# Performance work log

Hardware: AMD Instinct MI355X
Metric: run time of the kernel (lower is better)

The kernel has to match this reference:

```python
import jax, jax.numpy as jnp
import numpy as np
from jax.scipy.special import logsumexp

FEAT = 256; HEADS = 4; HDIM = FEAT // HEADS; LAYERS = 4
CLS = 3; S = 8; H, W = 400, 800; HC, WC = H // S, W // S
POS_FREQ = 10; VERTEX_THRESH = 0.015; BN_EPS = 1e-5
D_IN = 2 + 4 * POS_FREQ + 1 + CLS * S * S  # 235


def conv1d(x, Wt, b):
    # pointwise Conv1d: x [b,Cin,N] -> [b,Cout,N]
    return jnp.einsum('oi,bin->bon', Wt, x) + b[None, :, None]


def bnorm(x, p):
    # eval-mode BatchNorm1d over channel axis; p = stack([gamma,beta,mean,var]) [4,C]
    g, bt, mu, var = p[0], p[1], p[2], p[3]
    return g[None, :, None] * (x - mu[None, :, None]) * jax.lax.rsqrt(var[None, :, None] + BN_EPS) + bt[None, :, None]


def simple_nms(s, r):
    # max-pool NMS exactly as torch simple_nms (2 suppression rounds)
    def mp(x):
        return jax.lax.reduce_window(x, -jnp.inf, jax.lax.max,
                                     (1, 2 * r + 1, 2 * r + 1), (1, 1, 1), 'SAME')
    zeros = jnp.zeros_like(s)
    max_mask = s == mp(s)
    for _ in range(2):
        supp = mp(max_mask.astype(s.dtype)) > 0
        ss = jnp.where(supp, zeros, s)
        new_max = ss == mp(ss)
        max_mask = max_mask | (new_max & (~supp))
    return jnp.where(max_mask, s, zeros)


def pos_embed(nv):
    freqs = 2.0 ** jnp.linspace(0.0, POS_FREQ - 1.0, POS_FREQ)
    ang = nv[..., None, :] * freqs[None, None, :, None]          # [b,k,Pf,2]
    sc = jnp.concatenate([jnp.sin(ang), jnp.cos(ang)], -1)       # [b,k,Pf,4]
    return jnp.concatenate([nv, sc.reshape(nv.shape[0], nv.shape[1], -1)], -1)


def log_optimal_transport(scores, alpha, iters):
    b, m, n = scores.shape
    a = jnp.broadcast_to(alpha.reshape(1, 1, 1), (b, 1, 1)).astype(scores.dtype)
    couplings = jnp.concatenate([
        jnp.concatenate([scores, jnp.broadcast_to(a, (b, m, 1))], -1),
        jnp.concatenate([jnp.broadcast_to(a, (b, 1, n)), a], -1)], 1)
    ms, ns = float(m), float(n)
    norm = -np.log(ms + ns)
    log_mu = jnp.concatenate([jnp.full((m,), norm, scores.dtype),
                              jnp.array([np.log(ns) + norm], scores.dtype)])
    log_nu = jnp.concatenate([jnp.full((n,), norm, scores.dtype),
                              jnp.array([np.log(ms) + norm], scores.dtype)])
    log_mu = jnp.broadcast_to(log_mu[None], (b, m + 1))
    log_nu = jnp.broadcast_to(log_nu[None], (b, n + 1))

    @jax.checkpoint
    def step(carry, _):
        u, v = carry
        u = log_mu - logsumexp(couplings + v[:, None, :], axis=2)
        v = log_nu - logsumexp(couplings + u[:, :, None], axis=1)
        return (u, v), None

    (u, v), _ = jax.lax.scan(step, (jnp.zeros_like(log_mu), jnp.zeros_like(log_nu)), None, length=iters)
    return couplings + u[:, :, None] + v[:, None, :] - norm


def _forward(scores, distance, enc_W0, enc_b0, enc_bn, enc_W1, enc_b1,
             gnn_Wqkv, gnn_bqkv, gnn_Wm, gnn_bm, gnn_W1, gnn_b1, gnn_bn,
             gnn_W2, gnn_b2, final_W, final_b, alpha, k, nms_radius, sinkhorn_iters):
    b = scores.shape[0]
    s = simple_nms(scores, nms_radius)                        # [b,HC,WC]
    vals, idx = jax.lax.top_k(s.reshape(b, -1), k)            # fixed-k vertex selection
    mask = (vals > VERTEX_THRESH).astype(scores.dtype)        # [b,k] valid-vertex mask
    vy = idx // WC
    vx = idx % WC
    v_xy = jnp.stack([vx, vy], -1).astype(scores.dtype)       # (x,y) in coarse cells
    size = jnp.array([WC, HC], scores.dtype)
    nv = (v_xy - size / 2 + 0.5) / size                       # normalize_vertices
    pos = pos_embed(nv)                                       # [b,k,42]
    # sample_dt: distance-transform s*s patches per coarse cell, then gather
    dt = distance.reshape(b, CLS, HC, S, WC, S).transpose(0, 2, 4, 1, 3, 5).reshape(b, HC * WC, CLS * S * S)
    dtv = jnp.take_along_axis(dt, jnp.broadcast_to(idx[:, :, None], (b, k, CLS * S * S)), axis=1)
    emb = jnp.concatenate([pos, vals[..., None], dtv], -1)    # [b,k,235]
    # GraphEncoder MLP [235,256,256]
    x = emb.transpose(0, 2, 1)                                # [b,235,k]
    x = conv1d(x, enc_W0, enc_b0)
    x = jax.nn.relu(bnorm(x, enc_bn))
    x = conv1d(x, enc_W1, enc_b1)                             # [b,256,k]
    # AttentionalGNN (4 self-attention layers, 4 heads)
    scale = HDIM ** 0.5
    neg = jnp.asarray(-1e9, scores.dtype)
    m2 = (mask[:, None, :, None] * mask[:, None, None, :]) == 0   # [b,1,k,k]
    for l in range(LAYERS):
        q = conv1d(x, gnn_Wqkv[l, 0], gnn_bqkv[l, 0]).reshape(b, HDIM, HEADS, k)
        kk = conv1d(x, gnn_Wqkv[l, 1], gnn_bqkv[l, 1]).reshape(b, HDIM, HEADS, k)
        v = conv1d(x, gnn_Wqkv[l, 2], gnn_bqkv[l, 2]).reshape(b, HDIM, HEADS, k)
        att = jnp.einsum('bdhn,bdhm->bhnm', q, kk) / scale
        att = jnp.where(m2, neg, att)
        prob = jax.nn.softmax(att, axis=-1)
        msg = jnp.einsum('bhnm,bdhm->bdhn', prob, v).reshape(b, FEAT, k)
        msg = conv1d(msg, gnn_Wm[l], gnn_bm[l])
        y = jnp.concatenate([x, msg], axis=1)                 # [b,512,k]
        y = conv1d(y, gnn_W1[l], gnn_b1[l])
        y = jax.nn.relu(bnorm(y, gnn_bn[l]))
        y = conv1d(y, gnn_W2[l], gnn_b2[l])
        x = x + y
    md = conv1d(x, final_W, final_b)                          # final matching descriptors
    sc = jnp.einsum('bdn,bdm->bnm', md, md) / (FEAT ** 0.5)
    return log_optimal_transport(sc, alpha, sinkhorn_iters)   # [b,k+1,k+1]


def setup_inputs() -> dict:
    key = jax.random.key(0)
    ks = jax.random.split(key, 16)
    b, k = 4, 1024

    def w(kk, shape, fan_in):
        return (jax.random.normal(kk, shape, jnp.float32) / np.sqrt(fan_in)).astype(jnp.float32)

    def bn_params(kk, c, lead=()):
        k1, k2 = jax.random.split(kk)
        g = 1.0 + 0.1 * jax.random.normal(k1, lead + (c,), jnp.float32)
        bt = 0.1 * jax.random.normal(k2, lead + (c,), jnp.float32)
        mu = jnp.zeros(lead + (c,), jnp.float32)
        var = jnp.ones(lead + (c,), jnp.float32)
        return jnp.stack([g, bt, mu, var], axis=len(lead))

    return dict(
        scores=jax.random.uniform(ks[0], (b, HC, WC), jnp.float32),
        distance=jax.random.normal(ks[1], (b, CLS, H, W), jnp.float32),
        enc_W0=w(ks[2], (FEAT, D_IN), D_IN), enc_b0=jnp.zeros((FEAT,), jnp.float32),
        enc_bn=bn_params(ks[3], FEAT),
        enc_W1=w(ks[4], (FEAT, FEAT), FEAT), enc_b1=jnp.zeros((FEAT,), jnp.float32),
        gnn_Wqkv=w(ks[5], (LAYERS, 3, FEAT, FEAT), FEAT),
        gnn_bqkv=0.01 * jax.random.normal(ks[6], (LAYERS, 3, FEAT), jnp.float32),
        gnn_Wm=w(ks[7], (LAYERS, FEAT, FEAT), FEAT),
        gnn_bm=jnp.zeros((LAYERS, FEAT), jnp.float32),
        gnn_W1=w(ks[8], (LAYERS, 2 * FEAT, 2 * FEAT), 2 * FEAT),
        gnn_b1=jnp.zeros((LAYERS, 2 * FEAT), jnp.float32),
        gnn_bn=bn_params(ks[9], 2 * FEAT, (LAYERS,)),
        gnn_W2=w(ks[10], (LAYERS, FEAT, 2 * FEAT), 2 * FEAT),
        gnn_b2=jnp.zeros((LAYERS, FEAT), jnp.float32),
        final_W=w(ks[11], (FEAT, FEAT), FEAT),
        final_b=jnp.zeros((FEAT,), jnp.float32),
        alpha=jnp.ones((1,), jnp.float32),
        k=k, nms_radius=2, sinkhorn_iters=100,
    )


def reference(scores, distance, enc_W0, enc_b0, enc_bn, enc_W1, enc_b1,
              gnn_Wqkv, gnn_bqkv, gnn_Wm, gnn_bm, gnn_W1, gnn_b1, gnn_bn,
              gnn_W2, gnn_b2, final_W, final_b, alpha, k, nms_radius, sinkhorn_iters):
    return _forward(scores, distance, enc_W0, enc_b0, enc_bn, enc_W1, enc_b1,
                    gnn_Wqkv, gnn_bqkv, gnn_Wm, gnn_bm, gnn_W1, gnn_b1, gnn_bn,
                    gnn_W2, gnn_b2, final_W, final_b, alpha, k, nms_radius, sinkhorn_iters)
```

## Files before the change

### kernel.cpp

```cpp
#include <hip/hip_runtime.h>
#include <hip/hip_bf16.h>

typedef __hip_bfloat16 bf16;
typedef __attribute__((ext_vector_type(8))) short short8;
typedef __attribute__((ext_vector_type(4))) float f32x4;
typedef __attribute__((ext_vector_type(16))) float f32x16;
#define DEV __device__ __forceinline__

DEV float ldin(const void* p, long long i, int f) {
  return f ? ((const float*)p)[i]
           : __uint_as_float(((unsigned)((const unsigned short*)p)[i]) << 16);
}
DEV unsigned short f2bf(float x) {
  unsigned u = __float_as_uint(x);
  return (unsigned short)((u + 0x7FFFu + ((u >> 16) & 1u)) >> 16);
}
DEV float bf2f(unsigned short h) { return __uint_as_float((unsigned)h << 16); }

DEV void mp5f(const float* in, float* tmp, float* out, int t) {
  for (int i = t; i < 5000; i += 1024) {
    int y = i / 100, x = i % 100;
    int x0 = x - 2 < 0 ? 0 : x - 2, x1 = x + 2 > 99 ? 99 : x + 2;
    float m = -INFINITY;
    for (int xx = x0; xx <= x1; xx++) m = fmaxf(m, in[y * 100 + xx]);
    tmp[i] = m;
  }
  __syncthreads();
  for (int i = t; i < 5000; i += 1024) {
    int y = i / 100, x = i % 100;
    int y0 = y - 2 < 0 ? 0 : y - 2, y1 = y + 2 > 49 ? 49 : y + 2;
    float m = -INFINITY;
    for (int yy = y0; yy <= y1; yy++) m = fmaxf(m, tmp[yy * 100 + x]);
    out[i] = m;
  }
  __syncthreads();
}

__global__ __launch_bounds__(1024) void k_front(
    const void* __restrict__ scores, const void* __restrict__ dist,
    int* __restrict__ flagO, int* __restrict__ idxO, float* __restrict__ valsO,
    float* __restrict__ maskO, int* __restrict__ nvp) {
  extern __shared__ float lds[];
  float* S = lds;
  float* MK = lds + 5000;
  float* Z = lds + 10000;
  float* T = Z;
  float* P = Z + 5000;
  float* SP = Z + 10000;
  float* SS = Z + 15000;
  unsigned long long* keys = (unsigned long long*)(lds + 10000);
  __shared__ int bad, cnt;
  const int bb = blockIdx.x, t = threadIdx.x;
  if (t == 0) { bad = 0; cnt = 0; }
  __syncthreads();
  {
    int c = 0;
    const unsigned short* p = (const unsigned short*)dist;
    for (int i = t; i < 65536; i += 1024) {
      unsigned e = (p[i] >> 7) & 0xFF;
      if (e >= 0x86) c++;
    }
    atomicAdd(&bad, c);
  }
  __syncthreads();
  const int f = (bad > 100) ? 1 : 0;
  if (bb == 0 && t == 0) *flagO = f;
  for (int i = t; i < 5000; i += 1024) S[i] = ldin(scores, bb * 5000 + i, f);
  __syncthreads();
  mp5f(S, T, P, t);
  for (int i = t; i < 5000; i += 1024) MK[i] = (S[i] == P[i]) ? 1.f : 0.f;
  __syncthreads();
  for (int r = 0; r < 2; r++) {
    mp5f(MK, T, P, t);
    for (int i = t; i < 5000; i += 1024) {
      SP[i] = (P[i] > 0.f) ? 1.f : 0.f;
      SS[i] = (SP[i] != 0.f) ? 0.f : S[i];
    }
    __syncthreads();
    mp5f(SS, T, P, t);
    for (int i = t; i < 5000; i += 1024)
      if (MK[i] == 0.f) MK[i] = ((SS[i] == P[i]) && (SP[i] == 0.f)) ? 1.f : 0.f;
    __syncthreads();
  }
  for (int i = t; i < 8192; i += 1024) {
    unsigned long long kk;
    if (i < 5000) {
      float v = (MK[i] != 0.f) ? S[i] : 0.f;
      unsigned vb = __float_as_uint(v);
      kk = ((unsigned long long)vb << 32) | (unsigned)(0xFFFFFFFFu - (unsigned)i);
    } else {
      kk = 0ull;
    }
    keys[i] = ~kk;
  }
  __syncthreads();
  for (int k = 2; k <= 8192; k <<= 1) {
    for (int j = k >> 1; j > 0; j >>= 1) {
      for (int i = t; i < 8192; i += 1024) {
        int ixj = i ^ j;
        if (ixj > i) {
          unsigned long long a = keys[i], b = keys[ixj];
          bool up = ((i & k) == 0);
          if (up ? (a > b) : (a < b)) { keys[i] = b; keys[ixj] = a; }
        }
      }
      __syncthreads();
    }
  }
  {
    unsigned long long kk = ~keys[t];
    unsigned idx = 0xFFFFFFFFu - (unsigned)(kk & 0xFFFFFFFFu);
    float v = __uint_as_float((unsigned)(kk >> 32));
    idxO[bb * 1024 + t] = (int)idx;
    valsO[bb * 1024 + t] = v;
    bool valid = (v > 0.015f);
    maskO[bb * 1024 + t] = valid ? 1.f : 0.f;
    unsigned long long bal = __ballot(valid);
    if ((t & 63) == 0) atomicAdd(&cnt, (int)__popcll(bal));
  }
  __syncthreads();
  if (t == 0) nvp[bb] = cnt;
}

__global__ void k_prep(const void* __restrict__ W0, const void* __restrict__ W1e,
                       const void* __restrict__ Wqkv, const void* __restrict__ Wm,
                       const void* __restrict__ W1g, const void* __restrict__ W2g,
                       const void* __restrict__ Wf, unsigned short* __restrict__ WH,
                       unsigned short* __restrict__ WL, const int* __restrict__ flagp) {
  const int f = *flagp;
  long long g = (long long)blockIdx.x * 256 + threadIdx.x;
  float val;
  if (g < 65536) {
    int r = (int)(g >> 8), c = (int)(g & 255);
    val = (c < 235) ? ldin(W0, (long long)r * 235 + c, f) : 0.f;
  } else if (g < 131072) {
    val = ldin(W1e, g - 65536, f);
  } else if (g < 917504) {
    long long L = g - 131072;
    int R = (int)(L >> 8), k = (int)(L & 255);
    int l = R / 768, rp = R % 768;
    int qkv = rp >> 8, cp = rp & 255, h = cp >> 6, d = cp & 63;
    val = ldin(Wqkv, ((long long)((l * 3 + qkv) * 256 + d * 4 + h)) * 256 + k, f);
  } else if (g < 1179648) {
    long long L = g - 917504;
    int n = (int)(L >> 8), kp = (int)(L & 255);
    int k = (kp & 63) * 4 + (kp >> 6);
    val = ldin(Wm, (long long)n * 256 + k, f);
  } else if (g < 2228224) {
    val = ldin(W1g, g - 1179648, f);
  } else if (g < 2752512) {
    val = ldin(W2g, g - 2228224, f);
  } else {
    val = ldin(Wf, g - 2752512, f);
  }
  unsigned short h_ = f2bf(val);
  WH[g] = h_;
  WL[g] = f2bf(val - bf2f(h_));
}

__global__ void k_emb(const int* __restrict__ idxO, const float* __restrict__ valsO,
                      const void* __restrict__ distance,
                      unsigned short* __restrict__ eH, unsigned short* __restrict__ eL,
                      const int* __restrict__ flagp) {
  const int f = *flagp;
  const int vtx = blockIdx.x;
  const int bb = vtx >> 10, i = vtx & 1023;
  const int t = threadIdx.x;
  const int id = idxO[bb * 1024 + i];
  const int cy = id / 100, cx = id % 100;
  const float nvx = ((float)cx - 50.0f + 0.5f) / 100.0f;
  const float nvy = ((float)cy - 25.0f + 0.5f) / 50.0f;
  const int c = t;
  float val;
  if (c == 0) val = nvx;
  else if (c == 1) val = nvy;
  else if (c < 42) {
    int d = c - 2, fq = d >> 2, r = d & 3;
    float freq = (float)(1 << fq);
    float ang = ((r == 0 || r == 2) ? nvx : nvy) * freq;
    val = (r < 2) ? sinf(ang) : cosf(ang);
  } else if (c == 42) {
    val = valsO[bb * 1024 + i];
  } else if (c < 235) {
    int d = c - 43, cls = d >> 6, ii = (d >> 3) & 7, jj = d & 7;
    val = ldin(distance,
               (((long long)bb * 3 + cls) * 400 + (cy * 8 + ii)) * 800 + (cx * 8 + jj), f);
  } else {
    val = 0.f;
  }
  unsigned short h_ = f2bf(val);
  eH[(long long)vtx * 256 + c] = h_;
  eL[(long long)vtx * 256 + c] = f2bf(val - bf2f(h_));
}

template <int MODE, bool SPLIT, bool W3F>
__global__ __launch_bounds__(256) void gemm_pl(
    const unsigned short* __restrict__ Ah, const unsigned short* __restrict__ Al,
    const unsigned short* __restrict__ A2h, const unsigned short* __restrict__ A2l,
    int lda, const unsigned short* __restrict__ WHp,
    const unsigned short* __restrict__ WLp, const void* __restrict__ bias,
    const void* __restrict__ bn, float* __restrict__ CoutF,
    unsigned short* __restrict__ CoutH, unsigned short* __restrict__ CoutL,
    int ldc, int N, int K, float scale,
    long long aBatch, long long wBatch, long long cBatch,
    long long wOff, long long bOff, long long bnOff,
    const int* __restrict__ flagp) {
  const int rf = *flagp;
  const bool w3 = W3F || (rf != 0);
  const unsigned short* Ahp = Ah + (long long)blockIdx.z * aBatch;
  const unsigned short* Alp = Al + (long long)blockIdx.z * aBatch;
  CoutF += (long long)blockIdx.z * cBatch;
  const long long wb = wOff + (long long)blockIdx.z * wBatch;
  __shared__ unsigned short AH[2112], AL[2112], BH[2112], BL[2112];
  const int t = threadIdx.x;
  const int m0 = blockIdx.y * 64, n0 = blockIdx.x * 64;
  const int w = t >> 6, lane = t & 63, quad = lane >> 4, l15 = lane & 15;
  ushort4 rah[2], ral[2], rbh[2], rbl[2];
  auto loadT = [&](int k0) {
#pragma unroll
    for (int i = 0; i < 2; i++) {
      int id = t + (i << 8);
      int m = id >> 3, k4 = (id & 7) << 2;
      int kc = k0 + k4;
      const unsigned short* ph = Ahp;
      const unsigned short* pl = Alp;
      int kk = kc;
      if (SPLIT && kc >= 256) { ph = A2h; pl = A2l; kk = kc - 256; }
      long long ai = (long long)(m0 + m) * lda + kk;
      rah[i] = *(const ushort4*)&ph[ai];
      ral[i] = *(const ushort4*)&pl[ai];
      long long wi = wb + (long long)(n0 + m) * K + kc;
      rbh[i] = *(const ushort4*)&WHp[wi];
      rbl[i] = *(const ushort4*)&WLp[wi];
    }
  };
  auto storeT = [&]() {
#pragma unroll
    for (int i = 0; i < 2; i++) {
      int id = t + (i << 8);
      int m = id >> 3, k4 = (id & 7) << 2;
      int q = k4 >> 3, j0 = k4 & 7;
      int li = (q * 66 + m) * 8 + j0;
      *(ushort4*)&AH[li] = rah[i];
      *(ushort4*)&AL[li] = ral[i];
      *(ushort4*)&BH[li] = rbh[i];
      *(ushort4*)&BL[li] = rbl[i];
    }
  };
  f32x4 acc[4];
#pragma unroll
  for (int c = 0; c < 4; c++) acc[c] = (f32x4){0.f, 0.f, 0.f, 0.f};
  loadT(0);
  const int mr = w * 16 + l15;
  for (int k0 = 0; k0 < K; k0 += 32) {
    storeT();
    __syncthreads();
    if (k0 + 32 < K) loadT(k0 + 32);
    short8 fa = *(const short8*)&AH[(quad * 66 + mr) * 8];
    short8 fal = *(const short8*)&AL[(quad * 66 + mr) * 8];
#pragma unroll
    for (int cb = 0; cb < 4; cb++) {
      int nr = cb * 16 + l15;
      short8 fb = *(const short8*)&BH[(quad * 66 + nr) * 8];
      acc[cb] = __builtin_amdgcn_mfma_f32_16x16x32_bf16(fa, fb, acc[cb], 0, 0, 0);
      acc[cb] = __builtin_amdgcn_mfma_f32_16x16x32_bf16(fal, fb, acc[cb], 0, 0, 0);
      if (w3) {
        short8 fbl = *(const short8*)&BL[(quad * 66 + nr) * 8];
        acc[cb] = __builtin_amdgcn_mfma_f32_16x16x32_bf16(fa, fbl, acc[cb], 0, 0, 0);
      }
    }
    __syncthreads();
  }
#pragma unroll
  for (int cb = 0; cb < 4; cb++) {
    const int n = n0 + cb * 16 + l15;
    float bv = 0.f, g = 0.f, bt = 0.f, mu = 0.f, vr = 0.f;
    if (MODE != 4) {
      long long bidx;
      if (MODE == 3) {
        int c = n & 255;
        bidx = bOff + (long long)(n >> 8) * 256 + (c & 63) * 4 + (c >> 6);
      } else {
        bidx = bOff + n;
      }
      bv = ldin(bias, bidx, rf);
    }
    if (MODE == 1) {
      g = ldin(bn, bnOff + n, rf);
      bt = ldin(bn, bnOff + N + n, rf);
      mu = ldin(bn, bnOff + 2 * N + n, rf);
      vr = ldin(bn, bnOff + 3 * N + n, rf);
    }
#pragma unroll
    for (int r = 0; r < 4; r++) {
      const int m = m0 + w * 16 + quad * 4 + r;
      float v = acc[cb][r];
      if (MODE == 4) v *= scale;
      else v += bv;
      if (MODE == 1) {
        v = g * (v - mu) / sqrtf(vr + 1e-5f) + bt;
        v = fmaxf(v, 0.f);
      }
      if (MODE == 2) v += CoutF[(long long)m * ldc + n];
      if (MODE == 2 || MODE == 3 || MODE == 4 || MODE == 5)
        CoutF[(long long)m * ldc + n] = v;
      if (MODE == 0 || MODE == 1 || MODE == 2 || MODE == 5) {
        unsigned short hh = f2bf(v);
        CoutH[(long long)m * ldc + n] = hh;
        CoutL[(long long)m * ldc + n] = f2bf(v - bf2f(hh));
      }
    }
  }
}

__global__ __launch_bounds__(256) void k_attn(
    const float* __restrict__ QKV, const float* __restrict__ maskf,
    const int* __restrict__ nvp,
    unsigned short* __restrict__ msgH, unsigned short* __restrict__ msgL) {
  const int qt = blockIdx.x, h = blockIdx.y, bb = blockIdx.z;
  const int t = threadIdx.x;
  const int q2 = t >> 3, j8 = t & 7;
  __shared__ float Qst[64][68];
  __shared__ float Kst[64][68];
  __shared__ float Vs[64][72];
  __shared__ float Pst[64][68];
  __shared__ float qm[64], km[64];
  __shared__ float mvs[4][64];
  const float* Qb = QKV + (long long)bb * 1024 * 768 + h * 64;
  const float* Kb = Qb + 256;
  const float* Vb = Qb + 512;
  const int q0 = qt * 64;
  const int nv = nvp[bb];
  const int nt = (nv + 63) >> 6;
  float mi[2] = {-INFINITY, -INFINITY};
  float li[2] = {0.f, 0.f};
  float o[2][8] = {};
  const bool needMean = (q0 + 64 > nv);
  if (needMean) {
    const int c4 = t >> 6, d = t & 63;
    float s = 0.f;
    for (int r = c4 * 256; r < (c4 + 1) * 256; r++)
      s += Vb[(long long)r * 768 + d];
    mvs[c4][d] = s;
    __syncthreads();
  }
  if (q0 < nv) {
#pragma unroll
    for (int i = 0; i < 4; i++) {
      int id = t + i * 256;
      int q = id >> 4, d4 = (id & 15) << 2;
      float4 qv = *(const float4*)&Qb[(long long)(q0 + q) * 768 + d4];
      Qst[d4][q] = qv.x; Qst[d4 + 1][q] = qv.y;
      Qst[d4 + 2][q] = qv.z; Qst[d4 + 3][q] = qv.w;
    }
    if (t < 64) qm[t] = maskf[bb * 1024 + q0 + t];
    __syncthreads();
    const float qmr[2] = {qm[2 * q2], qm[2 * q2 + 1]};
    for (int kt = 0; kt < nt; kt++) {
      const int k0 = kt * 64;
      __syncthreads();
#pragma unroll
      for (int i = 0; i < 4; i++) {
        int id = t + i * 256;
        int n = id >> 4, d4 = (id & 15) << 2;
        float4 kv = *(const float4*)&Kb[(long long)(k0 + n) * 768 + d4];
        Kst[d4][n] = kv.x; Kst[d4 + 1][n] = kv.y;
        Kst[d4 + 2][n] = kv.z; Kst[d4 + 3][n] = kv.w;
        float4 vvv = *(const float4*)&Vb[(long long)(k0 + n) * 768 + d4];
        *(float4*)&Vs[n][d4] = vvv;
      }
      if (t < 64) km[t] = maskf[bb * 1024 + k0 + t];
      __syncthreads();
      float kmr[8];
#pragma unroll
      for (int kk = 0; kk < 8; kk++) kmr[kk] = km[8 * j8 + kk];
      float s[2][8] = {};
      for (int d = 0; d < 64; d++) {
        float2 qv = *(const float2*)&Qst[d][2 * q2];
        float4 ka = *(const float4*)&Kst[d][8 * j8];
        float4 kb = *(const float4*)&Kst[d][8 * j8 + 4];
        s[0][0] = fmaf(qv.x, ka.x, s[0][0]); s[0][1] = fmaf(qv.x, ka.y, s[0][1]);
        s[0][2] = fmaf(qv.x, ka.z, s[0][2]); s[0][3] = fmaf(qv.x, ka.w, s[0][3]);
        s[0][4] = fmaf(qv.x, kb.x, s[0][4]); s[0][5] = fmaf(qv.x, kb.y, s[0][5]);
        s[0][6] = fmaf(qv.x, kb.z, s[0][6]); s[0][7] = fmaf(qv.x, kb.w, s[0][7]);
        s[1][0] = fmaf(qv.y, ka.x, s[1][0]); s[1][1] = fmaf(qv.y, ka.y, s[1][1]);
        s[1][2] = fmaf(qv.y, ka.z, s[1][2]); s[1][3] = fmaf(qv.y, ka.w, s[1][3]);
        s[1][4] = fmaf(qv.y, kb.x, s[1][4]); s[1][5] = fmaf(qv.y, kb.y, s[1][5]);
        s[1][6] = fmaf(qv.y, kb.z, s[1][6]); s[1][7] = fmaf(qv.y, kb.w, s[1][7]);
      }
#pragma unroll
      for (int qq = 0; qq < 2; qq++) {
        float rm = -INFINITY;
#pragma unroll
        for (int kk = 0; kk < 8; kk++) {
          float val = (qmr[qq] * kmr[kk] == 0.f) ? -1e9f : s[qq][kk] * 0.125f;
          s[qq][kk] = val;
          rm = fmaxf(rm, val);
        }
        rm = fmaxf(rm, __shfl_xor(rm, 1));
        rm = fmaxf(rm, __shfl_xor(rm, 2));
        rm = fmaxf(rm, __shfl_xor(rm, 4));
        float nm = fmaxf(mi[qq], rm);
        float al = __expf(mi[qq] - nm);
        mi[qq] = nm;
        float sum = 0.f;
#pragma unroll
        for (int kk = 0; kk < 8; kk++) {
          float p = __expf(s[qq][kk] - nm);
          Pst[8 * j8 + kk][2 * q2 + qq] = p;
          sum += p;
        }
        sum += __shfl_xor(sum, 1);
        sum += __shfl_xor(sum, 2);
        sum += __shfl_xor(sum, 4);
        li[qq] = li[qq] * al + sum;
#pragma unroll
        for (int dd = 0; dd < 8; dd++) o[qq][dd] *= al;
      }
      __syncthreads();
      for (int m = 0; m < 64; m++) {
        float2 pv = *(const float2*)&Pst[m][2 * q2];
        float4 va = *(const float4*)&Vs[m][8 * j8];
        float4 vb = *(const float4*)&Vs[m][8 * j8 + 4];
        o[0][0] = fmaf(pv.x, va.x, o[0][0]); o[0][1] = fmaf(pv.x, va.y, o[0][1]);
        o[0][2] = fmaf(pv.x, va.z, o[0][2]); o[0][3] = fmaf(pv.x, va.w, o[0][3]);
        o[0][4] = fmaf(pv.x, vb.x, o[0][4]); o[0][5] = fmaf(pv.x, vb.y, o[0][5]);
        o[0][6] = fmaf(pv.x, vb.z, o[0][6]); o[0][7] = fmaf(pv.x, vb.w, o[0][7]);
        o[1][0] = fmaf(pv.y, va.x, o[1][0]); o[1][1] = fmaf(pv.y, va.y, o[1][1]);
        o[1][2] = fmaf(pv.y, va.z, o[1][2]); o[1][3] = fmaf(pv.y, va.w, o[1][3]);
        o[1][4] = fmaf(pv.y, vb.x, o[1][4]); o[1][5] = fmaf(pv.y, vb.y, o[1][5]);
        o[1][6] = fmaf(pv.y, vb.z, o[1][6]); o[1][7] = fmaf(pv.y, vb.w, o[1][7]);
      }
    }
  }
#pragma unroll
  for (int qq = 0; qq < 2; qq++) {
    const int q = q0 + 2 * q2 + qq;
    const long long idx = ((long long)bb * 1024 + q) * 256 + h * 64 + 8 * j8;
    const float inv = (q < nv) ? (1.f / li[qq]) : 0.f;
#pragma unroll
    for (int dd = 0; dd < 8; dd++) {
      int dp = 8 * j8 + dd;
      float val = (q < nv)
                      ? o[qq][dd] * inv
                      : (mvs[0][dp] + mvs[1][dp] + mvs[2][dp] + mvs[3][dp]) *
                            (1.f / 1024.f);
      unsigned short hh = f2bf(val);
      msgH[idx + dd] = hh;
      msgL[idx + dd] = f2bf(val - bf2f(hh));
    }
  }
}

__global__ __launch_bounds__(512, 1) void k_sinkhorn(
    const float* __restrict__ C, const void* __restrict__ alphap,
    unsigned long long* __restrict__ Ug, unsigned long long* __restrict__ Vg,
    void* __restrict__ outv, const int* __restrict__ flagp) {
  const int f = *flagp;
  const int bb = blockIdx.x >> 5;
  const int blk = blockIdx.x & 31;
  const int t = threadIdx.x;
  const int wid = t >> 6, lane = t & 63;
  const int rbase = (blk << 5) + (wid << 2);
  const float alpha = ldin(alphap, 0, f);
  const float* Cb = C + (long long)bb * 1050625;
  unsigned long long* Ub = Ug + bb * 1025;
  unsigned long long* Vb = Vg + bb * 1025;
  const float NORM = -7.624619086159398f;
  const float BIN = -0.6931471805599453f;
  __shared__ float sE[2][1025];
  __shared__ int convS[4];

  f32x16 ec0, ec1, ec2, ec3;
  float mc0, mc1, mc2, mc3;
  float ea0, ea1, ea2, ea3;
#define INIT_ROW(ECJ, MCJ, EAJ, J)                                       \
  {                                                                      \
    const float* cr = Cb + (long long)(rbase + (J)) * 1025;              \
    float mx = alpha;                \
    _Pragma("unroll") for (int i = 0; i < 16; i++) {                     \
      ECJ[i] = cr[(i << 6) + lane];                                      \
      mx = fmaxf(mx, ECJ[i]);                                            \
    }                                                                    \
    _Pragma("unroll") for (int o = 32; o; o >>= 1)                       \
        mx = fmaxf(mx, __shfl_xor(mx, o, 64));                           \
    MCJ = mx;                                                            \
    _Pragma("unroll") for (int i = 0; i < 16; i++)                       \
        ECJ[i] = __expf(ECJ[i] - mx);                                    \
    EAJ = __expf(alpha - mx);                                            \
  }
  INIT_ROW(ec0, mc0, ea0, 0)
  INIT_ROW(ec1, mc1, ea1, 1)
  INIT_ROW(ec2, mc2, ea2, 2)
  INIT_ROW(ec3, mc3, ea3, 3)
#undef INIT_ROW
  if (t < 4) convS[t] = 1;
  __syncthreads();

  float pu0 = 0.f, pu1 = 0.f, pu2 = 0.f, pu3 = 0.f;
  float pv0 = 0.f, pv1 = 0.f, pv2 = 0.f, pv3 = 0.f;
  float pAu = 0.f, pAv = 0.f;
  int prevAllc = 0;
  unsigned uW = 199u, vW = 200u;
  for (int half = 0; half < 200; half++) {
    const unsigned long long* src = (half & 1) ? Ub : Vb;
    unsigned long long* dst = (half & 1) ? Vb : Ub;
    float* sb = sE[half & 1];
    const unsigned want = (unsigned)half;
    unsigned long long d0, d1, d2 = ~0ull;
    for (;;) {
      d0 = __hip_atomic_load(src + 2 * t, __ATOMIC_RELAXED,
                             __HIP_MEMORY_SCOPE_AGENT);
      d1 = __hip_atomic_load(src + 2 * t + 1, __ATOMIC_RELAXED,
                             __HIP_MEMORY_SCOPE_AGENT);
      bool ok = (((unsigned)(d0 >> 32)) >> 1) >= want &&
                (((unsigned)(d1 >> 32)) >> 1) >= want;
      if (t == 0) {
        d2 = __hip_atomic_load(src + 1024, __ATOMIC_RELAXED,
                               __HIP_MEMORY_SCOPE_AGENT);
        ok = ok && ((((unsigned)(d2 >> 32)) >> 1) >= want);
      }
      if (ok) break;
      __builtin_amdgcn_s_sleep(1);
    }
    {
      unsigned cb = (unsigned)(d0 >> 32) & (unsigned)(d1 >> 32) &
                    (unsigned)(d2 >> 32);
      if (!(cb & 1u)) convS[half & 3] = 0;
    }
    sb[2 * t] = __expf(__uint_as_float((unsigned)d0));
    sb[2 * t + 1] = __expf(__uint_as_float((unsigned)d1));
    if (t == 0) sb[1024] = __expf(__uint_as_float((unsigned)d2));
    __syncthreads();
    const int allc = convS[half & 3];
    if ((half & 1) == 0 && half >= 48 && allc && prevAllc) {
      uW = (unsigned)(half - 1);
      vW = (unsigned)half;
      break;
    }
    prevAllc = allc;
    if (t == 0) convS[(half + 2) & 3] = 1;
    f32x16 svr;
#pragma unroll
    for (int i = 0; i < 16; i++) svr[i] = sb[(i << 6) + lane];
    const float ea = sb[1024];
    float dsts0, dsts1, dsts2, dsts3;
#define ROW_SUM(ECJ, MCJ, EAJ, OUT)                                      \
  {                                                                      \
    float s = 0.f;                                                       \
    _Pragma("unroll") for (int i = 0; i < 16; i++)                       \
        s = fmaf(ECJ[i], svr[i], s);                                     \
    _Pragma("unroll") for (int o = 32; o; o >>= 1)                       \
        s += __shfl_xor(s, o, 64);                                       \
    s = fmaf(EAJ, ea, s);                                                \
    OUT = NORM - (MCJ + __logf(s));                                      \
  }
    ROW_SUM(ec0, mc0, ea0, dsts0)
    ROW_SUM(ec1, mc1, ea1, dsts1)
    ROW_SUM(ec2, mc2, ea2, dsts2)
    ROW_SUM(ec3, mc3, ea3, dsts3)
#undef ROW_SUM
    float wd;
    if (half & 1) {
      wd = fmaxf(fmaxf(fabsf(dsts0 - pv0), fabsf(dsts1 - pv1)),
                 fmaxf(fabsf(dsts2 - pv2), fabsf(dsts3 - pv3)));
      pv0 = dsts0; pv1 = dsts1; pv2 = dsts2; pv3 = dsts3;
    } else {
      wd = fmaxf(fmaxf(fabsf(dsts0 - pu0), fabsf(dsts1 - pu1)),
                 fmaxf(fabsf(dsts2 - pu2), fabsf(dsts3 - pu3)));
      pu0 = dsts0; pu1 = dsts1; pu2 = dsts2; pu3 = dsts3;
    }
    const unsigned st = ((unsigned)(half + 1) << 1) | (wd < 4e-3f ? 1u : 0u);
    const unsigned long long shi = (unsigned long long)st << 32;
    if (lane < 4) {
      float myv = (lane & 2) ? ((lane & 1) ? dsts3 : dsts2)
                             : ((lane & 1) ? dsts1 : dsts0);
      __hip_atomic_store(dst + rbase + lane, shi | __float_as_uint(myv),
                         __ATOMIC_RELAXED, __HIP_MEMORY_SCOPE_AGENT);
    }
    if (blk == 0 && wid == 0) {
      float sa = 0.f;
#pragma unroll
      for (int i = 0; i < 16; i++) sa += svr[i];
#pragma unroll
      for (int o = 32; o; o >>= 1) sa += __shfl_xor(sa, o, 64);
      sa += ea;
      float nval = BIN - (alpha + __logf(sa));
      float pA = (half & 1) ? pAv : pAu;
      float wdA = fabsf(nval - pA);
      if (half & 1) pAv = nval; else pAu = nval;
      unsigned stA = ((unsigned)(half + 1) << 1) | (wdA < 4e-3f ? 1u : 0u);
      if (lane == 0)
        __hip_atomic_store(dst + 1024,
                           ((unsigned long long)stA << 32) | __float_as_uint(nval),
                           __ATOMIC_RELAXED, __HIP_MEMORY_SCOPE_AGENT);
    }
  }
  __shared__ float su[1025], svf[1025];
  for (int i = t; i < 1025; i += 512) {
    for (;;) {
      unsigned long long d = __hip_atomic_load(Ub + i, __ATOMIC_RELAXED,
                                               __HIP_MEMORY_SCOPE_AGENT);
      if ((((unsigned)(d >> 32)) >> 1) >= uW) {
        su[i] = __uint_as_float((unsigned)d);
        break;
      }
      __builtin_amdgcn_s_sleep(2);
    }
    for (;;) {
      unsigned long long d = __hip_atomic_load(Vb + i, __ATOMIC_RELAXED,
                                               __HIP_MEMORY_SCOPE_AGENT);
      if ((((unsigned)(d >> 32)) >> 1) >= vW) {
        svf[i] = __uint_as_float((unsigned)d);
        break;
      }
      __builtin_amdgcn_s_sleep(2);
    }
  }
  __syncthreads();
  const long long base = (long long)bb * 1050625;
  const int r0g = blk << 5;
  for (int i = t; i < 32800; i += 512) {
    int r = i / 1025, cc = i - r * 1025;
    float cv = Cb[(long long)r0g * 1025 + i];
    if (cc == 1024) cv = alpha;
    float val = cv + su[r0g + r] + svf[cc] - NORM;
    if (f) ((float*)outv)[base + (long long)r0g * 1025 + i] = val;
    else ((bf16*)outv)[base + (long long)r0g * 1025 + i] = __float2bfloat16(val);
  }
  if (blk == 0) {
    const float un = su[1024];
    for (int cc = t; cc < 1025; cc += 512) {
      float val = alpha + un + svf[cc] - NORM;
      if (f) ((float*)outv)[base + (long long)1024 * 1025 + cc] = val;
      else ((bf16*)outv)[base + (long long)1024 * 1025 + cc] = __float2bfloat16(val);
    }
  }
}

extern "C" void kernel_launch(void* const* d_in, const int* in_sizes, int n_in,
                              void* d_out, int out_size, void* d_ws, size_t ws_size,
                              hipStream_t stream) {
  const void* scores = d_in[0];
  const void* distance = d_in[1];
  const void* enc_W0 = d_in[2];
  const void* enc_b0 = d_in[3];
  const void* enc_bn = d_in[4];
  const void* enc_W1 = d_in[5];
  const void* enc_b1 = d_in[6];
  const void* gnn_Wqkv = d_in[7];
  const void* gnn_bqkv = d_in[8];
  const void* gnn_Wm = d_in[9];
  const void* gnn_bm = d_in[10];
  const void* gnn_W1 = d_in[11];
  const void* gnn_b1 = d_in[12];
  const void* gnn_bn = d_in[13];
  const void* gnn_W2 = d_in[14];
  const void* gnn_b2 = d_in[15];
  const void* final_W = d_in[16];
  const void* final_b = d_in[17];
  const void* alpha = d_in[18];
  (void)in_sizes; (void)n_in; (void)out_size; (void)ws_size;

  char* ws = (char*)d_ws;
  size_t off = 0;
  auto alloc = [&](size_t bytes) -> void* {
    void* p = ws + off;
    off += (bytes + 255) & ~(size_t)255;
    return p;
  };
  typedef unsigned short ush;
  int* flag = (int*)alloc(256);
  int* nvA = (int*)alloc(256);
  int* idxO = (int*)alloc(4096 * 4);
  float* valsO = (float*)alloc(4096 * 4);
  float* maskO = (float*)alloc(4096 * 4);
  ush* WH = (ush*)alloc((size_t)2818048 * 2);
  ush* WL = (ush*)alloc((size_t)2818048 * 2);
  ush* embH = (ush*)alloc((size_t)1048576 * 2);
  ush* embL = (ush*)alloc((size_t)1048576 * 2);
  ush* T0H = (ush*)alloc((size_t)1048576 * 2);
  ush* T0L = (ush*)alloc((size_t)1048576 * 2);
  ush* XH = (ush*)alloc((size_t)1048576 * 2);
  ush* XL = (ush*)alloc((size_t)1048576 * 2);
  float* Xf = (float*)alloc((size_t)1048576 * 4);
  float* QKVf = (float*)alloc((size_t)3145728 * 4);
  ush* msgH = (ush*)alloc((size_t)1048576 * 2);
  ush* msgL = (ush*)alloc((size_t)1048576 * 2);
  ush* M2H = (ush*)alloc((size_t)1048576 * 2);
  ush* M2L = (ush*)alloc((size_t)1048576 * 2);
  ush* Y1H = (ush*)alloc((size_t)2097152 * 2);
  ush* Y1L = (ush*)alloc((size_t)2097152 * 2);
  ush* MDH = (ush*)alloc((size_t)1048576 * 2);
  ush* MDL = (ush*)alloc((size_t)1048576 * 2);
  float* Cpl = (float*)alloc((size_t)4 * 1050625 * 4);
  unsigned long long* Ubuf = (unsigned long long*)alloc((size_t)4 * 1025 * 8);
  unsigned long long* Vbuf = (unsigned long long*)alloc((size_t)4 * 1025 * 8);

  hipMemsetAsync(Ubuf, 0, (size_t)4 * 1025 * 8, stream);
  hipMemsetAsync(Vbuf, 0, (size_t)4 * 1025 * 8, stream);

  static bool attrSet = false;
  if (!attrSet) {
    hipFuncSetAttribute(reinterpret_cast<const void*>(&k_front),
                        hipFuncAttributeMaxDynamicSharedMemorySize, 120000);
    attrSet = true;
  }

  const dim3 b256(256);
  k_front<<<4, 1024, 120000, stream>>>(scores, distance, flag, idxO, valsO,
                                       maskO, nvA);
  k_prep<<<11008, b256, 0, stream>>>(enc_W0, enc_W1, gnn_Wqkv, gnn_Wm, gnn_W1,
                                     gnn_W2, final_W, WH, WL, flag);
  k_emb<<<4096, b256, 0, stream>>>(idxO, valsO, distance, embH, embL, flag);

  gemm_pl<1, false, false><<<dim3(4, 64, 1), b256, 0, stream>>>(
      embH, embL, nullptr, nullptr, 256, WH + 0, WL + 0, enc_b0, enc_bn,
      nullptr, T0H, T0L, 256, 256, 256, 1.f, 0, 0, 0, 0, 0, 0, flag);
  gemm_pl<5, false, false><<<dim3(4, 64, 1), b256, 0, stream>>>(
      T0H, T0L, nullptr, nullptr, 256, WH + 65536, WL + 65536, enc_b1, nullptr,
      Xf, XH, XL, 256, 256, 256, 1.f, 0, 0, 0, 0, 0, 0, flag);

  for (int l = 0; l < 4; l++) {
    gemm_pl<3, false, false><<<dim3(12, 64, 1), b256, 0, stream>>>(
        XH, XL, nullptr, nullptr, 256, WH + 131072, WL + 131072, gnn_bqkv,
        nullptr, QKVf, nullptr, nullptr, 768, 768, 256, 1.f, 0, 0, 0,
        (long long)l * 196608, (long long)l * 768, 0, flag);
    k_attn<<<dim3(16, 4, 4), b256, 0, stream>>>(QKVf, maskO, nvA, msgH, msgL);
    gemm_pl<0, false, false><<<dim3(4, 64, 1), b256, 0, stream>>>(
        msgH, msgL, nullptr, nullptr, 256, WH + 917504, WL + 917504, gnn_bm,
        nullptr, nullptr, M2H, M2L, 256, 256, 256, 1.f, 0, 0, 0,
        (long long)l * 65536, (long long)l * 256, 0, flag);
    gemm_pl<1, true, false><<<dim3(8, 64, 1), b256, 0, stream>>>(
        XH, XL, M2H, M2L, 256, WH + 1179648, WL + 1179648, gnn_b1, gnn_bn,
        nullptr, Y1H, Y1L, 512, 512, 512, 1.f, 0, 0, 0,
        (long long)l * 262144, (long long)l * 512, (long long)l * 2048, flag);
    gemm_pl<2, false, false><<<dim3(4, 64, 1), b256, 0, stream>>>(
        Y1H, Y1L, nullptr, nullptr, 512, WH + 2228224, WL + 2228224, gnn_b2,
        nullptr, Xf, XH, XL, 256, 256, 512, 1.f, 0, 0, 0,
        (long long)l * 131072, (long long)l * 256, 0, flag);
  }
  gemm_pl<0, false, false><<<dim3(4, 64, 1), b256, 0, stream>>>(
      XH, XL, nullptr, nullptr, 256, WH + 2752512, WL + 2752512, final_b,
      nullptr, nullptr, MDH, MDL, 256, 256, 256, 1.f, 0, 0, 0, 0, 0, 0, flag);
  gemm_pl<4, false, true><<<dim3(16, 16, 4), b256, 0, stream>>>(
      MDH, MDL, nullptr, nullptr, 256, MDH, MDL, nullptr, nullptr, Cpl, nullptr,
      nullptr, 1025, 1024, 256, 0.0625f, 262144, 262144, 1050625, 0, 0, 0, flag);
  k_sinkhorn<<<128, 512, 0, stream>>>(Cpl, alpha, Ubuf, Vbuf, d_out, flag);
}
```

Before: 1.408 ms.

## Compact NMS peaks before sorting and sort only a 1024-element bitonic network

After NMS, surviving peaks are stream-compacted into the key buffer with an atomic counter. When there are at most 1024 of them, a single-pass 1024-wide bitonic sort replaces the full 8192-element sort. The remaining output slots are then filled with non-peak indices in ascending order, using a block prefix scan, to reproduce the tie order of the original. If more than 1024 peaks survive, the old full sort is used instead. A small risk remains: peaks whose score is exactly zero may not tie-break against non-peaks the same way the original did.

```diff
diff --git a/kernel.cpp b/kernel.cpp
--- a/kernel.cpp
+++ b/kernel.cpp
@@ -49,9 +49,10 @@
   float* SP = Z + 10000;
   float* SS = Z + 15000;
   unsigned long long* keys = (unsigned long long*)(lds + 10000);
-  __shared__ int bad, cnt;
+  int* sc = (int*)(lds + 26384);
+  __shared__ int bad, cnt, npkS;
   const int bb = blockIdx.x, t = threadIdx.x;
-  if (t == 0) { bad = 0; cnt = 0; }
+  if (t == 0) { bad = 0; cnt = 0; npkS = 0; }
   __syncthreads();
   {
     int c = 0;
@@ -82,41 +83,108 @@
       if (MK[i] == 0.f) MK[i] = ((SS[i] == P[i]) && (SP[i] == 0.f)) ? 1.f : 0.f;
     __syncthreads();
   }
-  for (int i = t; i < 8192; i += 1024) {
-    unsigned long long kk;
-    if (i < 5000) {
-      float v = (MK[i] != 0.f) ? S[i] : 0.f;
-      unsigned vb = __float_as_uint(v);
-      kk = ((unsigned long long)vb << 32) | (unsigned)(0xFFFFFFFFu - (unsigned)i);
-    } else {
-      kk = 0ull;
-    }
-    keys[i] = ~kk;
-  }
-  __syncthreads();
-  for (int k = 2; k <= 8192; k <<= 1) {
-    for (int j = k >> 1; j > 0; j >>= 1) {
-      for (int i = t; i < 8192; i += 1024) {
-        int ixj = i ^ j;
-        if (ixj > i) {
-          unsigned long long a = keys[i], b = keys[ixj];
-          bool up = ((i & k) == 0);
-          if (up ? (a > b) : (a < b)) { keys[i] = b; keys[ixj] = a; }
+  for (int i = t; i < 5000; i += 1024)
+    if (MK[i] != 0.f) {
+      int pos = atomicAdd(&npkS, 1);
+      unsigned long long kk =
+          ((unsigned long long)__float_as_uint(S[i]) << 32) |
+          (unsigned)(0xFFFFFFFFu - (unsigned)i);
+      keys[pos] = ~kk;
+    }
+  __syncthreads();
+  const int npk = npkS;
+  if (npk <= 1024) {
+    if (t >= npk) keys[t] = ~0ull;
+    __syncthreads();
+    for (int k = 2; k <= 1024; k <<= 1) {
+      for (int j = k >> 1; j > 0; j >>= 1) {
+        int ixj = t ^ j;
+        if (ixj > t) {
+          unsigned long long a = keys[t], b = keys[ixj];
+          bool up = ((t & k) == 0);
+          if (up ? (a > b) : (a < b)) { keys[t] = b; keys[ixj] = a; }
         }
-      }
+        __syncthreads();
+      }
+    }
+    if (t < npk) {
+      unsigned long long kk = ~keys[t];
+      unsigned idx = 0xFFFFFFFFu - (unsigned)(kk & 0xFFFFFFFFu);
+      float v = __uint_as_float((unsigned)(kk >> 32));
+      idxO[bb * 1024 + t] = (int)idx;
+      valsO[bb * 1024 + t] = v;
+      bool valid = (v > 0.015f);
+      maskO[bb * 1024 + t] = valid ? 1.f : 0.f;
+      unsigned long long bal = __ballot(valid);
+      if ((t & 63) == 0) atomicAdd(&cnt, (int)__popcll(bal));
+    }
+    const int ibase = t * 5;
+    int c0 = 0;
+#pragma unroll
+    for (int q = 0; q < 5; q++) {
+      int i = ibase + q;
+      if (i < 5000 && MK[i] == 0.f) c0++;
+    }
+    sc[t] = c0;
+    __syncthreads();
+    for (int off = 1; off < 1024; off <<= 1) {
+      int v = (t >= off) ? sc[t - off] : 0;
       __syncthreads();
-    }
-  }
-  {
-    unsigned long long kk = ~keys[t];
-    unsigned idx = 0xFFFFFFFFu - (unsigned)(kk & 0xFFFFFFFFu);
-    float v = __uint_as_float((unsigned)(kk >> 32));
-    idxO[bb * 1024 + t] = (int)idx;
-    valsO[bb * 1024 + t] = v;
-    bool valid = (v > 0.015f);
-    maskO[bb * 1024 + t] = valid ? 1.f : 0.f;
-    unsigned long long bal = __ballot(valid);
-    if ((t & 63) == 0) atomicAdd(&cnt, (int)__popcll(bal));
+      sc[t] += v;
+      __syncthreads();
+    }
+    int rank = sc[t] - c0;
+#pragma unroll
+    for (int q = 0; q < 5; q++) {
+      int i = ibase + q;
+      if (i < 5000 && MK[i] == 0.f) {
+        int pos = npk + rank;
+        if (pos < 1024) {
+          idxO[bb * 1024 + pos] = i;
+          valsO[bb * 1024 + pos] = 0.f;
+          maskO[bb * 1024 + pos] = 0.f;
+        }
+        rank++;
+      }
+    }
+  } else {
+    for (int i = t; i < 8192; i += 1024) {
+      unsigned long long kk;
+      if (i < 5000) {
+        float v = (MK[i] != 0.f) ? S[i] : 0.f;
+        unsigned vb = __float_as_uint(v);
+        kk = ((unsigned long long)vb << 32) |
+             (unsigned)(0xFFFFFFFFu - (unsigned)i);
+      } else {
+        kk = 0ull;
+      }
+      keys[i] = ~kk;
+    }
+    __syncthreads();
+    for (int k = 2; k <= 8192; k <<= 1) {
+      for (int j = k >> 1; j > 0; j >>= 1) {
+        for (int i = t; i < 8192; i += 1024) {
+          int ixj = i ^ j;
+          if (ixj > i) {
+            unsigned long long a = keys[i], b = keys[ixj];
+            bool up = ((i & k) == 0);
+            if (up ? (a > b) : (a < b)) { keys[i] = b; keys[ixj] = a; }
+          }
+        }
+        __syncthreads();
+      }
+    }
+    {
+      unsigned long long kk = ~keys[t];
+      unsigned idx = 0xFFFFFFFFu - (unsigned)(kk & 0xFFFFFFFFu);
+      float v = __uint_as_float((unsigned)(kk >> 32));
+      idxO[bb * 1024 + t] = (int)idx;
+      valsO[bb * 1024 + t] = v;
+      bool valid = (v > 0.015f);
+      maskO[bb * 1024 + t] = valid ? 1.f : 0.f;
+      unsigned long long bal = __ballot(valid);
+      if ((t & 63) == 0) atomicAdd(&cnt, (int)__popcll(bal));
+    }
   }
   __syncthreads();
   if (t == 0) nvp[bb] = cnt;
```

After: 1.313 ms. -6.7%, faster.
